# Performance work log

Measured on AMD Instinct MI355X. Metric: run time of the kernel, lower is better.

Reference implementation:

```python
import jax, jax.numpy as jnp
import numpy as np
import math

B, T, D = 2, 2048, 512      # batch, n_tp, input_dim
DM, H = 64, 16              # per-head d_model, nhead


def setup_inputs() -> dict:
    key = jax.random.key(0)
    ks = jax.random.split(key, 12)
    s = 0.02
    return {
        "data": jax.random.normal(ks[0], (B, T, D), jnp.float32),
        "mask": jax.random.uniform(ks[1], (B, T, D), jnp.float32),
        "wq": jax.random.normal(ks[2], (D, DM * H), jnp.float32) * s,
        "bq": jnp.zeros((DM * H,), jnp.float32),
        "wk": jax.random.normal(ks[3], (D, DM * H), jnp.float32) * s,
        "bk": jnp.zeros((DM * H,), jnp.float32),
        "wv": jax.random.normal(ks[4], (D, DM * H), jnp.float32) * s,
        "bv": jnp.zeros((DM * H,), jnp.float32),
        "wo": jax.random.normal(ks[5], (DM * H, D), jnp.float32) * s,
        "bo": jnp.zeros((D,), jnp.float32),
    }


def reference(data, mask, wq, bq, wk, bk, wv, bv, wo, bo):
    b, t, d = data.shape
    # NOTE: torch code splits proj as (d_model, nhead): head index is fastest-varying
    def split_heads(x):  # [b,t,DM*H] -> [b,H,t,DM]
        return x.reshape(b, t, DM, H).transpose(0, 3, 1, 2)

    q = split_heads(data @ wq + bq)
    k = split_heads(data @ wk + bk)
    v = split_heads(data @ wv + bv)

    scores = jnp.einsum("bhqd,bhkd->bhqk", q, k) / math.sqrt(DM)
    # padded key positions: rows of mask that sum to exactly 0
    pad = (jnp.sum(mask, axis=-1) == 0.0)  # [b, t] (key axis)
    scores = jnp.where(pad[:, None, None, :], -1e9, scores)
    attn = jax.nn.softmax(scores, axis=-1)  # dropout = identity (eval mode)
    out = jnp.einsum("bhqk,bhkd->bhqd", attn, v)
    # merge as (nhead, d_model) — matches torch permute(0,2,1,3).reshape
    out = out.transpose(0, 2, 1, 3).reshape(b, t, H * DM)
    return out @ wo + bo
```

## Files before the change

kernel.cpp:

```cpp
#include <hip/hip_runtime.h>
#include <hip/hip_bf16.h>

#define B_  2
#define T_  2048
#define D_  512
#define DM_ 64
#define H_  16
#define NQ_ (DM_*H_)
#define NT_ (T_/64)

typedef __bf16 bf16x8 __attribute__((ext_vector_type(8)));
typedef __bf16 bf16x4 __attribute__((ext_vector_type(4)));
typedef float  f32x4  __attribute__((ext_vector_type(4)));
typedef unsigned int u32;

static __device__ __forceinline__ __bf16 bfc(float x) { return (__bf16)x; }
static __device__ __forceinline__ unsigned short f2bf(float x) {
    __bf16 b = (__bf16)x;
    unsigned short u;
    __builtin_memcpy(&u, &b, 2);
    return u;
}

#if __has_builtin(__builtin_amdgcn_exp2f)
static __device__ __forceinline__ float EXP2(float x) { return __builtin_amdgcn_exp2f(x); }
#else
static __device__ __forceinline__ float EXP2(float x) {
    float r; asm("v_exp_f32 %0, %1\ns_nop 0" : "=v"(r) : "v"(x)); return r;
}
#endif

#define GLOAD16(gp, lp) \
    __builtin_amdgcn_global_load_lds((const __attribute__((address_space(1))) u32*)(gp), \
                                     (__attribute__((address_space(3))) u32*)(lp), 16, 0, 0)

__global__ __launch_bounds__(256)
void prep_kernel(const float* __restrict__ mask, float* __restrict__ padb,
                 const float* __restrict__ data, unsigned short* __restrict__ dataB,
                 const float* __restrict__ wq, const float* __restrict__ wk,
                 const float* __restrict__ wv, unsigned short* __restrict__ btall,
                 const float* __restrict__ wo, unsigned short* __restrict__ wot)
{
    __shared__ float t[32][33];
    const int bid = blockIdx.x;
    const int tid = threadIdx.x;
    if (bid < 1024) {
        const int row  = bid * 4 + (tid >> 6);
        const int lane = tid & 63;
        const float* p = mask + (size_t)row * D_;
        float4 a = *(const float4*)&p[lane * 8];
        float4 b = *(const float4*)&p[lane * 8 + 4];
        float s = a.x + a.y + a.z + a.w + b.x + b.y + b.z + b.w;
#pragma unroll
        for (int off = 32; off; off >>= 1) s += __shfl_down(s, off);
        if (lane == 0) padb[row] = (s == 0.0f) ? -1e9f : 0.0f;
    } else if (bid < 2048) {
        int i = ((bid - 1024) * 256 + tid) * 8;
        float4 a = *(const float4*)&data[i];
        float4 b = *(const float4*)&data[i + 4];
        bf16x8 u = {bfc(a.x), bfc(a.y), bfc(a.z), bfc(a.w),
                    bfc(b.x), bfc(b.y), bfc(b.z), bfc(b.w)};
        *(bf16x8*)&dataB[i] = u;
    } else if (bid < 3584) {
        const int idx = bid - 2048;
        const int z = idx >> 9, rem = idx & 511;
        const int c0 = (rem & 31) * 32, r0 = (rem >> 5) * 32;
        const float* in = (z == 0) ? wq : (z == 1) ? wk : wv;
        unsigned short* out = btall + (size_t)z * NQ_ * D_;
        const int tx = tid & 31, ty = tid >> 5;
#pragma unroll
        for (int i = 0; i < 4; ++i)
            t[ty * 4 + i][tx] = in[(size_t)(r0 + ty * 4 + i) * NQ_ + c0 + tx];
        __syncthreads();
#pragma unroll
        for (int i = 0; i < 4; ++i)
            out[(size_t)(c0 + ty * 4 + i) * D_ + r0 + tx] = f2bf(t[tx][ty * 4 + i]);
    } else {
        const int idx = bid - 3584;
        const int c0 = (idx & 15) * 32, r0 = (idx >> 4) * 32;
        const int tx = tid & 31, ty = tid >> 5;
#pragma unroll
        for (int i = 0; i < 4; ++i)
            t[ty * 4 + i][tx] = wo[(size_t)(r0 + ty * 4 + i) * D_ + c0 + tx];
        __syncthreads();
#pragma unroll
        for (int i = 0; i < 4; ++i)
            wot[(size_t)(c0 + ty * 4 + i) * NQ_ + r0 + tx] = f2bf(t[tx][ty * 4 + i]);
    }
}

__global__ __launch_bounds__(256)
void mgemm_qkv_kernel(const unsigned short* __restrict__ A,
                      const unsigned short* __restrict__ BtAll,
                      const float* __restrict__ bq, const float* __restrict__ bk,
                      const float* __restrict__ bv,
                      unsigned short* __restrict__ Qh, unsigned short* __restrict__ Kh,
                      unsigned short* __restrict__ Vt, float alpha_q)
{
    const int K = D_;
    __shared__ __align__(16) unsigned short Al[2][128 * 64];
    __shared__ __align__(16) unsigned short Bl[2][128 * 64];

    const int tid = threadIdx.x;
    const int w  = tid >> 6, l = tid & 63;
    const int lo = l & 15,  g = l >> 4;
    const int wri = w >> 1, wci = w & 1;
    const int m0 = blockIdx.y * 128, n0 = blockIdx.x * 128;
    const int lrow = l >> 3;
    const int lslot = (l & 7) ^ lrow;

    f32x4 acc[4][4] = {};
    const int nk = K >> 6;

#pragma unroll
    for (int p = 0; p < 4; ++p) {
        int br = w * 32 + p * 8;
        GLOAD16(A     + (size_t)(m0 + br + lrow) * K + lslot * 8, (char*)Al[0] + br * 128);
        GLOAD16(BtAll + (size_t)(n0 + br + lrow) * K + lslot * 8, (char*)Bl[0] + br * 128);
    }
    __syncthreads();

    for (int t = 0; t < nk; ++t) {
        const int cur = t & 1;
        if (t + 1 < nk) {
            const int k0 = (t + 1) << 6;
#pragma unroll
            for (int p = 0; p < 4; ++p) {
                int br = w * 32 + p * 8;
                GLOAD16(A     + (size_t)(m0 + br + lrow) * K + k0 + lslot * 8,
                        (char*)Al[cur ^ 1] + br * 128);
                GLOAD16(BtAll + (size_t)(n0 + br + lrow) * K + k0 + lslot * 8,
                        (char*)Bl[cur ^ 1] + br * 128);
            }
        }
#pragma unroll
        for (int kk = 0; kk < 2; ++kk) {
            bf16x8 af[4], bfr[4];
#pragma unroll
            for (int i = 0; i < 4; ++i) {
                int row = wri * 64 + i * 16 + lo;
                af[i] = *(const bf16x8*)&Al[cur][row * 64 + ((((kk << 2) + g) ^ (row & 7)) << 3)];
                int col = wci * 64 + i * 16 + lo;
                bfr[i] = *(const bf16x8*)&Bl[cur][col * 64 + ((((kk << 2) + g) ^ (col & 7)) << 3)];
            }
#pragma unroll
            for (int i = 0; i < 4; ++i)
#pragma unroll
                for (int j = 0; j < 4; ++j)
                    acc[i][j] = __builtin_amdgcn_mfma_f32_16x16x32_bf16(af[i], bfr[j], acc[i][j], 0, 0, 0);
        }
        __syncthreads();
    }

    const int seg = n0 >> 10;
    const int n0l = n0 & 1023;
    const float* bias = (seg == 0) ? bq : (seg == 1) ? bk : bv;
    const float alpha = (seg == 0) ? alpha_q : 1.0f;
    unsigned short* o16 = (seg == 0) ? Qh : (seg == 1) ? Kh : Vt;

    const int mb = m0 + wri * 64 + g * 4;
    float bb[4];
#pragma unroll
    for (int j = 0; j < 4; ++j) bb[j] = bias[n0l + wci * 64 + j * 16 + lo];
    const int head = lo;
    const int dmb  = (n0l >> 4) + wci * 4;
    if (seg < 2) {
#pragma unroll
        for (int i = 0; i < 4; ++i)
#pragma unroll
            for (int jj = 0; jj < 4; ++jj) {
                int m = mb + i * 16 + jj;
                int t = m & (T_ - 1), bidx = m >> 11;
                bf16x4 u = {bfc((acc[i][0][jj] + bb[0]) * alpha),
                            bfc((acc[i][1][jj] + bb[1]) * alpha),
                            bfc((acc[i][2][jj] + bb[2]) * alpha),
                            bfc((acc[i][3][jj] + bb[3]) * alpha)};
                *(bf16x4*)&o16[(((size_t)(bidx * H_ + head)) * T_ + t) * DM_ + dmb] = u;
            }
    } else {
#pragma unroll
        for (int i = 0; i < 4; ++i)
#pragma unroll
            for (int j = 0; j < 4; ++j) {
                int m = mb + i * 16;
                int t = m & (T_ - 1), bidx = m >> 11;
                bf16x4 u = {bfc(acc[i][j][0] + bb[j]), bfc(acc[i][j][1] + bb[j]),
                            bfc(acc[i][j][2] + bb[j]), bfc(acc[i][j][3] + bb[j])};
                *(bf16x4*)&o16[((size_t)(bidx * H_ + head) * DM_ + dmb + j) * T_ + t] = u;
            }
    }
}

__global__ __launch_bounds__(256)
void mgemm_out_kernel(const unsigned short* __restrict__ A,
                      const unsigned short* __restrict__ Bt,
                      const float* __restrict__ bias, float* __restrict__ out,
                      int M, int N, int K)
{
    __shared__ __align__(16) unsigned short Al[2][64 * 64];
    __shared__ __align__(16) unsigned short Bl[2][128 * 64];

    const int tid = threadIdx.x;
    const int w  = tid >> 6, l = tid & 63;
    const int lo = l & 15,  g = l >> 4;
    const int wri = w >> 1, wci = w & 1;
    const int m0 = blockIdx.y * 64, n0 = blockIdx.x * 128;
    const int lrow = l >> 3;
    const int lslot = (l & 7) ^ lrow;

    f32x4 acc[2][4] = {};
    const int nk = K >> 6;

#pragma unroll
    for (int p = 0; p < 2; ++p) {
        int br = w * 16 + p * 8;
        GLOAD16(A + (size_t)(m0 + br + lrow) * K + lslot * 8, (char*)Al[0] + br * 128);
    }
#pragma unroll
    for (int p = 0; p < 4; ++p) {
        int br = w * 32 + p * 8;
        GLOAD16(Bt + (size_t)(n0 + br + lrow) * K + lslot * 8, (char*)Bl[0] + br * 128);
    }
    __syncthreads();

    for (int t = 0; t < nk; ++t) {
        const int cur = t & 1;
        if (t + 1 < nk) {
            const int k0 = (t + 1) << 6;
#pragma unroll
            for (int p = 0; p < 2; ++p) {
                int br = w * 16 + p * 8;
                GLOAD16(A + (size_t)(m0 + br + lrow) * K + k0 + lslot * 8,
                        (char*)Al[cur ^ 1] + br * 128);
            }
#pragma unroll
            for (int p = 0; p < 4; ++p) {
                int br = w * 32 + p * 8;
                GLOAD16(Bt + (size_t)(n0 + br + lrow) * K + k0 + lslot * 8,
                        (char*)Bl[cur ^ 1] + br * 128);
            }
        }
#pragma unroll
        for (int kk = 0; kk < 2; ++kk) {
            bf16x8 af[2], bfr[4];
#pragma unroll
            for (int i = 0; i < 2; ++i) {
                int row = wri * 32 + i * 16 + lo;
                af[i] = *(const bf16x8*)&Al[cur][row * 64 + ((((kk << 2) + g) ^ (row & 7)) << 3)];
            }
#pragma unroll
            for (int j = 0; j < 4; ++j) {
                int col = wci * 64 + j * 16 + lo;
                bfr[j] = *(const bf16x8*)&Bl[cur][col * 64 + ((((kk << 2) + g) ^ (col & 7)) << 3)];
            }
#pragma unroll
            for (int i = 0; i < 2; ++i)
#pragma unroll
                for (int j = 0; j < 4; ++j)
                    acc[i][j] = __builtin_amdgcn_mfma_f32_16x16x32_bf16(af[i], bfr[j], acc[i][j], 0, 0, 0);
        }
        __syncthreads();
    }

    const int mb = m0 + wri * 32 + g * 4;
#pragma unroll
    for (int j = 0; j < 4; ++j) {
        int n = n0 + wci * 64 + j * 16 + lo;
        float bb = bias[n];
#pragma unroll
        for (int i = 0; i < 2; ++i)
#pragma unroll
            for (int jj = 0; jj < 4; ++jj) {
                int m = mb + i * 16 + jj;
                out[(size_t)m * N + n] = acc[i][j][jj] + bb;
            }
    }
}

__global__ __launch_bounds__(256, 2)
void attn_kernel(const unsigned short* __restrict__ Qh,
                 const unsigned short* __restrict__ Kh,
                 const unsigned short* __restrict__ Vt,
                 const float* __restrict__ padb,
                 unsigned short* __restrict__ ctx)
{
    __shared__ __align__(16) unsigned short Ks[2][64 * 64];
    __shared__ __align__(16) unsigned short Vs[3][64 * 64];
    __shared__ __align__(16) unsigned short Ps[4][2][32 * 64];
    __shared__ __align__(16) float pbs[T_];

    const int tid  = threadIdx.x;
    const int w    = tid >> 6;
    const int l    = tid & 63;
    const int lo16 = l & 15;
    const int g    = l >> 4;
    const int lrow = l >> 3;
    const int lslot = (l & 7) ^ lrow;

    const int f   = blockIdx.x;
    const int s   = f >> 3;
    const int bh  = (f & 7) * 4 + (s >> 4);
    const int q0  = (s & 15) * 128;
    const int bb  = bh >> 4;
    const int hh  = bh & 15;

    bf16x8 qf[2][2];
#pragma unroll
    for (int qt = 0; qt < 2; ++qt) {
        const unsigned short* Qp =
            Qh + ((size_t)bh * T_ + q0 + w * 32 + qt * 16 + lo16) * DM_ + g * 8;
        qf[qt][0] = *(const bf16x8*)(Qp);
        qf[qt][1] = *(const bf16x8*)(Qp + 32);
    }

    const unsigned short* kgp =
        Kh + (size_t)bh * T_ * DM_ + (size_t)(w * 16 + lrow) * DM_ + lslot * 8;
    const unsigned short* vgp =
        Vt + (size_t)bh * DM_ * T_ + (size_t)(w * 16 + lrow) * T_ + lslot * 8;

    {
        const float* src = padb + bb * T_ + tid * 8;
        *(float4*)&pbs[tid * 8]     = *(const float4*)(src);
        *(float4*)&pbs[tid * 8 + 4] = *(const float4*)(src + 4);
    }

    GLOAD16(kgp,           (char*)Ks[0] + (w * 16) * 128);
    GLOAD16(kgp + 8 * DM_, (char*)Ks[0] + (w * 16 + 8) * 128);
    GLOAD16(vgp,           (char*)Vs[0] + (w * 16) * 128);
    GLOAD16(vgp + 8 * T_,  (char*)Vs[0] + (w * 16 + 8) * 128);
    kgp += 64 * DM_;
    vgp += 64;

    const int rswz = (lo16 & 7) << 4;
    __syncthreads();

    f32x4 oa[2][4] = {};
    f32x4 ls4[2] = {};
    const float* pbp = pbs;

    char* Kc = (char*)Ks[0];
    char* Kw = (char*)Ks[1];
    char* Vr = (char*)Vs[2];
    char* Vn = (char*)Vs[0];
    char* Vw = (char*)Vs[1];
    char* Pc = (char*)&Ps[w][0][0];
    char* Pp = (char*)&Ps[w][1][0];

    {
        GLOAD16(kgp,           Kw + (w * 16) * 128);
        GLOAD16(kgp + 8 * DM_, Kw + (w * 16 + 8) * 128);
        GLOAD16(vgp,           Vw + (w * 16) * 128);
        GLOAD16(vgp + 8 * T_,  Vw + (w * 16 + 8) * 128);
        kgp += 64 * DM_;
        vgp += 64;

        f32x4 sa[2][4];
#pragma unroll
        for (int nt = 0; nt < 4; ++nt) {
            f32x4 pb4 = *(const f32x4*)&pbp[nt * 16 + g * 4];
            sa[0][nt] = pb4;
            sa[1][nt] = pb4;
        }
        __builtin_amdgcn_s_setprio(1);
#pragma unroll
        for (int ks = 0; ks < 2; ++ks) {
#pragma unroll
            for (int nt = 0; nt < 4; ++nt) {
                int row = nt * 16 + lo16;
                int off = (row * 128 + ks * 64 + g * 16) ^ ((row & 7) << 4);
                bf16x8 kf = *(const bf16x8*)(Kc + off);
#pragma unroll
                for (int qt = 0; qt < 2; ++qt)
                    sa[qt][nt] = __builtin_amdgcn_mfma_f32_16x16x32_bf16(kf, qf[qt][ks], sa[qt][nt], 0, 0, 0);
            }
        }
        __builtin_amdgcn_s_setprio(0);
#pragma unroll
        for (int qt = 0; qt < 2; ++qt) {
            const int prow = qt * 16 + lo16;
#pragma unroll
            for (int nt = 0; nt < 4; ++nt) {
                float e0 = EXP2(sa[qt][nt][0]);
                float e1 = EXP2(sa[qt][nt][1]);
                float e2 = EXP2(sa[qt][nt][2]);
                float e3 = EXP2(sa[qt][nt][3]);
                ls4[qt] += (f32x4){e0, e1, e2, e3};
                bf16x4 p4 = {bfc(e0), bfc(e1), bfc(e2), bfc(e3)};
                int wb = (prow * 128 + nt * 32 + g * 8) ^ rswz;
                *(bf16x4*)(Pc + wb) = p4;
            }
        }
        pbp += 64;
        __syncthreads();
        { char* tk = Kc; Kc = Kw; Kw = tk;
          char* tv = Vr; Vr = Vn; Vn = Vw; Vw = tv;
          char* tp = Pc; Pc = Pp; Pp = tp; }
    }

    for (int it = 1; it < NT_; ++it) {
        if (it + 1 < NT_) {
            GLOAD16(kgp,           Kw + (w * 16) * 128);
            GLOAD16(kgp + 8 * DM_, Kw + (w * 16 + 8) * 128);
            GLOAD16(vgp,           Vw + (w * 16) * 128);
            GLOAD16(vgp + 8 * T_,  Vw + (w * 16 + 8) * 128);
            kgp += 64 * DM_;
            vgp += 64;
        }

        f32x4 sa[2][4];
#pragma unroll
        for (int nt = 0; nt < 4; ++nt) {
            f32x4 pb4 = *(const f32x4*)&pbp[nt * 16 + g * 4];
            sa[0][nt] = pb4;
            sa[1][nt] = pb4;
        }
        __builtin_amdgcn_s_setprio(1);
#pragma unroll
        for (int ks = 0; ks < 2; ++ks) {
#pragma unroll
            for (int nt = 0; nt < 4; ++nt) {
                int row = nt * 16 + lo16;
                int off = (row * 128 + ks * 64 + g * 16) ^ ((row & 7) << 4);
                bf16x8 kf = *(const bf16x8*)(Kc + off);
#pragma unroll
                for (int qt = 0; qt < 2; ++qt)
                    sa[qt][nt] = __builtin_amdgcn_mfma_f32_16x16x32_bf16(kf, qf[qt][ks], sa[qt][nt], 0, 0, 0);
            }
        }
        __builtin_amdgcn_s_setprio(0);

        bf16x8 pf[2][2];
#pragma unroll
        for (int qt = 0; qt < 2; ++qt)
#pragma unroll
            for (int ks = 0; ks < 2; ++ks) {
                int poff = ((qt * 16 + lo16) * 128 + ks * 64 + g * 16) ^ rswz;
                pf[qt][ks] = *(const bf16x8*)(Pp + poff);
            }
        bf16x8 vf[2][4];
#pragma unroll
        for (int ks = 0; ks < 2; ++ks)
#pragma unroll
            for (int nd = 0; nd < 4; ++nd) {
                int row = nd * 16 + lo16;
                int off = (row * 128 + ks * 64 + g * 16) ^ ((row & 7) << 4);
                vf[ks][nd] = *(const bf16x8*)(Vr + off);
            }

#pragma unroll
        for (int qt = 0; qt < 2; ++qt) {
            const int prow = qt * 16 + lo16;
#pragma unroll
            for (int nt = 0; nt < 4; ++nt) {
                float e0 = EXP2(sa[qt][nt][0]);
                float e1 = EXP2(sa[qt][nt][1]);
                float e2 = EXP2(sa[qt][nt][2]);
                float e3 = EXP2(sa[qt][nt][3]);
                ls4[qt] += (f32x4){e0, e1, e2, e3};
                bf16x4 p4 = {bfc(e0), bfc(e1), bfc(e2), bfc(e3)};
                int wb = (prow * 128 + nt * 32 + g * 8) ^ rswz;
                *(bf16x4*)(Pc + wb) = p4;
            }
        }

        __builtin_amdgcn_s_setprio(1);
#pragma unroll
        for (int ks = 0; ks < 2; ++ks)
#pragma unroll
            for (int nd = 0; nd < 4; ++nd)
#pragma unroll
                for (int qt = 0; qt < 2; ++qt)
                    oa[qt][nd] = __builtin_amdgcn_mfma_f32_16x16x32_bf16(vf[ks][nd], pf[qt][ks], oa[qt][nd], 0, 0, 0);
        __builtin_amdgcn_s_setprio(0);

        pbp += 64;
        __syncthreads();
        { char* tk = Kc; Kc = Kw; Kw = tk;
          char* tv = Vr; Vr = Vn; Vn = Vw; Vw = tv;
          char* tp = Pc; Pc = Pp; Pp = tp; }
    }

    {
#pragma unroll
        for (int ks = 0; ks < 2; ++ks) {
            bf16x8 pf[2];
#pragma unroll
            for (int qt = 0; qt < 2; ++qt) {
                int poff = ((qt * 16 + lo16) * 128 + ks * 64 + g * 16) ^ rswz;
                pf[qt] = *(const bf16x8*)(Pp + poff);
            }
#pragma unroll
            for (int nd = 0; nd < 4; ++nd) {
                int row = nd * 16 + lo16;
                int off = (row * 128 + ks * 64 + g * 16) ^ ((row & 7) << 4);
                bf16x8 vfl = *(const bf16x8*)(Vr + off);
#pragma unroll
                for (int qt = 0; qt < 2; ++qt)
                    oa[qt][nd] = __builtin_amdgcn_mfma_f32_16x16x32_bf16(vfl, pf[qt], oa[qt][nd], 0, 0, 0);
            }
        }
    }

#pragma unroll
    for (int qt = 0; qt < 2; ++qt) {
        float lt = (ls4[qt][0] + ls4[qt][1]) + (ls4[qt][2] + ls4[qt][3]);
        lt += __shfl_xor(lt, 16);
        lt += __shfl_xor(lt, 32);
        float linv = 1.0f / lt;
        const size_t crow =
            ((size_t)(bb * T_ + q0 + w * 32 + qt * 16 + lo16)) * NQ_ + hh * DM_;
#pragma unroll
        for (int nd = 0; nd < 4; ++nd) {
            bf16x4 u = {bfc(oa[qt][nd][0] * linv), bfc(oa[qt][nd][1] * linv),
                        bfc(oa[qt][nd][2] * linv), bfc(oa[qt][nd][3] * linv)};
            *(bf16x4*)&ctx[crow + nd * 16 + g * 4] = u;
        }
    }
}

extern "C" void kernel_launch(void* const* d_in, const int* in_sizes, int n_in,
                              void* d_out, int out_size, void* d_ws, size_t ws_size,
                              hipStream_t stream) {
    const float* data = (const float*)d_in[0];
    const float* mask = (const float*)d_in[1];
    const float* wq   = (const float*)d_in[2];
    const float* bq   = (const float*)d_in[3];
    const float* wk   = (const float*)d_in[4];
    const float* bk   = (const float*)d_in[5];
    const float* wv   = (const float*)d_in[6];
    const float* bv   = (const float*)d_in[7];
    const float* wo   = (const float*)d_in[8];
    const float* bo   = (const float*)d_in[9];
    float* out = (float*)d_out;

    char* ws = (char*)d_ws;
    const size_t MB = 1024 * 1024;
    unsigned short* Qh    = (unsigned short*)(ws);
    unsigned short* Kh    = (unsigned short*)(ws +  8 * MB);
    unsigned short* Vt    = (unsigned short*)(ws + 16 * MB);
    unsigned short* CTX   = (unsigned short*)(ws + 24 * MB);
    unsigned short* dataB = (unsigned short*)(ws + 32 * MB);
    unsigned short* BtAll = (unsigned short*)(ws + 36 * MB);
    unsigned short* wot   = (unsigned short*)(ws + 39 * MB);
    float*          padb  = (float*)         (ws + 40 * MB);

    const int M = B_ * T_;
    const float alpha_q = 0.125f * 1.44269504089f;

    prep_kernel<<<4096, 256, 0, stream>>>(mask, padb, data, dataB,
                                          wq, wk, wv, BtAll, wo, wot);

    mgemm_qkv_kernel<<<dim3(3 * NQ_ / 128, M / 128), 256, 0, stream>>>(
        dataB, BtAll, bq, bk, bv, Qh, Kh, Vt, alpha_q);

    attn_kernel<<<512, 256, 0, stream>>>(Qh, Kh, Vt, padb, CTX);

    mgemm_out_kernel<<<dim3(D_ / 128, M / 64), 256, 0, stream>>>(
        CTX, wot, bo, out, M, D_, NQ_);
}
```

Measured before the change: 109.2 us.

## Interleave softmax exp with PV MFMAs and prefetch pad bias into registers

New measurement: 105.4 us. 3.5% less time.

```diff
diff --git a/kernel.cpp b/kernel.cpp
--- a/kernel.cpp
+++ b/kernel.cpp
@@ -287,7 +287,6 @@
     __shared__ __align__(16) unsigned short Ks[2][64 * 64];
     __shared__ __align__(16) unsigned short Vs[3][64 * 64];
     __shared__ __align__(16) unsigned short Ps[4][2][32 * 64];
-    __shared__ __align__(16) float pbs[T_];
 
     const int tid  = threadIdx.x;
     const int w    = tid >> 6;
@@ -317,12 +316,11 @@
         Kh + (size_t)bh * T_ * DM_ + (size_t)(w * 16 + lrow) * DM_ + lslot * 8;
     const unsigned short* vgp =
         Vt + (size_t)bh * DM_ * T_ + (size_t)(w * 16 + lrow) * T_ + lslot * 8;
-
-    {
-        const float* src = padb + bb * T_ + tid * 8;
-        *(float4*)&pbs[tid * 8]     = *(const float4*)(src);
-        *(float4*)&pbs[tid * 8 + 4] = *(const float4*)(src + 4);
-    }
+    const float* pbase = padb + bb * T_ + g * 4;
+
+    f32x4 pbc[4];
+#pragma unroll
+    for (int nt = 0; nt < 4; ++nt) pbc[nt] = *(const f32x4*)(pbase + nt * 16);
 
     GLOAD16(kgp,           (char*)Ks[0] + (w * 16) * 128);
     GLOAD16(kgp + 8 * DM_, (char*)Ks[0] + (w * 16 + 8) * 128);
@@ -336,7 +334,6 @@
 
     f32x4 oa[2][4] = {};
     f32x4 ls4[2] = {};
-    const float* pbp = pbs;
 
     char* Kc = (char*)Ks[0];
     char* Kw = (char*)Ks[1];
@@ -347,6 +344,10 @@
     char* Pp = (char*)&Ps[w][1][0];
 
     {
+        f32x4 pbn[4];
+#pragma unroll
+        for (int nt = 0; nt < 4; ++nt)
+            pbn[nt] = *(const f32x4*)(pbase + 64 + nt * 16);
         GLOAD16(kgp,           Kw + (w * 16) * 128);
         GLOAD16(kgp + 8 * DM_, Kw + (w * 16 + 8) * 128);
         GLOAD16(vgp,           Vw + (w * 16) * 128);
@@ -357,9 +358,8 @@
         f32x4 sa[2][4];
 #pragma unroll
         for (int nt = 0; nt < 4; ++nt) {
-            f32x4 pb4 = *(const f32x4*)&pbp[nt * 16 + g * 4];
-            sa[0][nt] = pb4;
-            sa[1][nt] = pb4;
+            sa[0][nt] = pbc[nt];
+            sa[1][nt] = pbc[nt];
         }
         __builtin_amdgcn_s_setprio(1);
 #pragma unroll
@@ -390,7 +390,8 @@
                 *(bf16x4*)(Pc + wb) = p4;
             }
         }
-        pbp += 64;
+#pragma unroll
+        for (int nt = 0; nt < 4; ++nt) pbc[nt] = pbn[nt];
         __syncthreads();
         { char* tk = Kc; Kc = Kw; Kw = tk;
           char* tv = Vr; Vr = Vn; Vn = Vw; Vw = tv;
@@ -398,7 +399,11 @@
     }
 
     for (int it = 1; it < NT_; ++it) {
+        f32x4 pbn[4];
         if (it + 1 < NT_) {
+#pragma unroll
+            for (int nt = 0; nt < 4; ++nt)
+                pbn[nt] = *(const f32x4*)(pbase + (it + 1) * 64 + nt * 16);
             GLOAD16(kgp,           Kw + (w * 16) * 128);
             GLOAD16(kgp + 8 * DM_, Kw + (w * 16 + 8) * 128);
             GLOAD16(vgp,           Vw + (w * 16) * 128);
@@ -410,9 +415,8 @@
         f32x4 sa[2][4];
 #pragma unroll
         for (int nt = 0; nt < 4; ++nt) {
-            f32x4 pb4 = *(const f32x4*)&pbp[nt * 16 + g * 4];
-            sa[0][nt] = pb4;
-            sa[1][nt] = pb4;
+            sa[0][nt] = pbc[nt];
+            sa[1][nt] = pbc[nt];
         }
         __builtin_amdgcn_s_setprio(1);
 #pragma unroll
@@ -448,32 +452,25 @@
             }
 
 #pragma unroll
-        for (int qt = 0; qt < 2; ++qt) {
-            const int prow = qt * 16 + lo16;
-#pragma unroll
-            for (int nt = 0; nt < 4; ++nt) {
-                float e0 = EXP2(sa[qt][nt][0]);
-                float e1 = EXP2(sa[qt][nt][1]);
-                float e2 = EXP2(sa[qt][nt][2]);
-                float e3 = EXP2(sa[qt][nt][3]);
-                ls4[qt] += (f32x4){e0, e1, e2, e3};
-                bf16x4 p4 = {bfc(e0), bfc(e1), bfc(e2), bfc(e3)};
-                int wb = (prow * 128 + nt * 32 + g * 8) ^ rswz;
-                *(bf16x4*)(Pc + wb) = p4;
-            }
-        }
-
-        __builtin_amdgcn_s_setprio(1);
-#pragma unroll
-        for (int ks = 0; ks < 2; ++ks)
-#pragma unroll
-            for (int nd = 0; nd < 4; ++nd)
-#pragma unroll
-                for (int qt = 0; qt < 2; ++qt)
-                    oa[qt][nd] = __builtin_amdgcn_mfma_f32_16x16x32_bf16(vf[ks][nd], pf[qt][ks], oa[qt][nd], 0, 0, 0);
-        __builtin_amdgcn_s_setprio(0);
-
-        pbp += 64;
+        for (int c = 0; c < 8; ++c) {
+            const int qt = c >> 2, nt = c & 3;
+            float e0 = EXP2(sa[qt][nt][0]);
+            float e1 = EXP2(sa[qt][nt][1]);
+            float e2 = EXP2(sa[qt][nt][2]);
+            float e3 = EXP2(sa[qt][nt][3]);
+            ls4[qt] += (f32x4){e0, e1, e2, e3};
+            bf16x4 p4 = {bfc(e0), bfc(e1), bfc(e2), bfc(e3)};
+            int wb = ((qt * 16 + lo16) * 128 + nt * 32 + g * 8) ^ rswz;
+            *(bf16x4*)(Pc + wb) = p4;
+            const int ks = c >> 2, nd = c & 3;
+            oa[0][nd] = __builtin_amdgcn_mfma_f32_16x16x32_bf16(vf[ks][nd], pf[0][ks], oa[0][nd], 0, 0, 0);
+            oa[1][nd] = __builtin_amdgcn_mfma_f32_16x16x32_bf16(vf[ks][nd], pf[1][ks], oa[1][nd], 0, 0, 0);
+        }
+
+        if (it + 1 < NT_) {
+#pragma unroll
+            for (int nt = 0; nt < 4; ++nt) pbc[nt] = pbn[nt];
+        }
         __syncthreads();
         { char* tk = Kc; Kc = Kw; Kw = tk;
           char* tv = Vr; Vr = Vn; Vn = Vw; Vw = tv;
```
